# Optimization experiments

Hardware: AMD Instinct MI355X
Metric: run time of the kernel (lower is better)

Reference implementation:

```python
import jax, jax.numpy as jnp
import numpy as np

B, N, C = 4, 1370, 1024
H, DH = 16, C // 16
N_ROPE = 1369  # patch tokens covered by RoPE (prefix=1 CLS token)


def _rotate_half(x):
    x1, x2 = jnp.split(x, 2, axis=-1)
    return jnp.concatenate([-x2, x1], axis=-1)


def _rope_apply(x, sin, cos):
    return x * cos + _rotate_half(x) * sin


def setup_inputs() -> dict:
    key = jax.random.key(0)
    ks = jax.random.split(key, 7)
    return {
        "x": jax.random.normal(ks[0], (B, N, C), dtype=jnp.float32),
        "sin": jax.random.normal(ks[1], (N_ROPE, DH), dtype=jnp.float32),
        "cos": jax.random.normal(ks[2], (N_ROPE, DH), dtype=jnp.float32),
        "w_qkv": jax.random.normal(ks[3], (C, 3 * C), dtype=jnp.float32) * (C ** -0.5),
        "b_qkv": jax.random.normal(ks[4], (3 * C,), dtype=jnp.float32) * 0.02,
        "w_proj": jax.random.normal(ks[5], (C, C), dtype=jnp.float32) * (C ** -0.5),
        "b_proj": jax.random.normal(ks[6], (C,), dtype=jnp.float32) * 0.02,
    }


def reference(x, sin, cos, w_qkv, b_qkv, w_proj, b_proj):
    b, n, c = x.shape
    # QKV projection -> [3, B, H, N, DH]
    qkv = (x @ w_qkv + b_qkv).reshape(b, n, 3, H, DH).transpose(2, 0, 3, 1, 4)
    q, k, v = qkv[0], qkv[1], qkv[2]
    # RoPE on the last N_ROPE tokens (prefix tokens, e.g. CLS, left untouched)
    prefix = n - sin.shape[-2]
    q = jnp.concatenate([q[:, :, :prefix, :], _rope_apply(q[:, :, prefix:, :], sin, cos)], axis=-2)
    k = jnp.concatenate([k[:, :, :prefix, :], _rope_apply(k[:, :, prefix:, :], sin, cos)], axis=-2)
    # Full attention
    scale = 1.0 / jnp.sqrt(jnp.asarray(DH, dtype=x.dtype))
    attn = jnp.einsum('bhqd,bhkd->bhqk', q, k) * scale
    attn = jax.nn.softmax(attn, axis=-1)
    out = jnp.einsum('bhqk,bhkd->bhqd', attn, v)
    out = out.transpose(0, 2, 1, 3).reshape(b, n, c)
    return out @ w_proj + b_proj
```

## Files before the change

### kernel.cpp

```cpp
#include <hip/hip_runtime.h>
#include <hip/hip_bf16.h>

#define B_ 4
#define N_ 1370
#define C_ 1024
#define H_ 16
#define DH_ 64
#define NR_ 1369
#define M_ (B_*N_)
#define VTS_ 1408
#define ALS 64
#define PLS 72

#define QSCALE 0.1803368801111f

typedef _Float16 f16x8  __attribute__((ext_vector_type(8)));
typedef __bf16   bf16x8 __attribute__((ext_vector_type(8)));
typedef float    f32x4  __attribute__((ext_vector_type(4)));

__device__ __forceinline__ f16x8 ld_frag_h(const unsigned short* p) {
    uint4 u = *(const uint4*)p;
    return __builtin_bit_cast(f16x8, u);
}
__device__ __forceinline__ bf16x8 ld_frag_b(const unsigned short* p) {
    uint4 u = *(const uint4*)p;
    return __builtin_bit_cast(bf16x8, u);
}
__device__ __forceinline__ unsigned short f2h(float f) {
    _Float16 h = (_Float16)f;
    return __builtin_bit_cast(unsigned short, h);
}
__device__ __forceinline__ unsigned short f2bf(float f) {
    __hip_bfloat16 h = __float2bfloat16(f);
    return __builtin_bit_cast(unsigned short, h);
}
__device__ __forceinline__ bf16x8 ones_bf() {
    uint4 u = make_uint4(0x3F803F80u, 0x3F803F80u, 0x3F803F80u, 0x3F803F80u);
    return __builtin_bit_cast(bf16x8, u);
}

__device__ __forceinline__ void load_lds16(const unsigned short* g, unsigned short* l) {
    __builtin_amdgcn_global_load_lds(
        (const __attribute__((address_space(1))) unsigned int*)g,
        (__attribute__((address_space(3))) unsigned int*)l,
        16, 0, 0);
}

__global__ __launch_bounds__(256)
void conv_x_k(const float* __restrict__ x, unsigned short* __restrict__ xo, int total4) {
    int i = blockIdx.x * 256 + threadIdx.x;
    if (i >= total4) return;
    float4 v = ((const float4*)x)[i];
    ushort4 h;
    h.x = f2h(v.x); h.y = f2h(v.y); h.z = f2h(v.z); h.w = f2h(v.w);
    ((ushort4*)xo)[i] = h;
}

__global__ __launch_bounds__(256)
void conv_wt_k(const float* __restrict__ w, unsigned short* __restrict__ wt, int Ncol) {
    __shared__ unsigned short Th[64][68];
    const int tid = threadIdx.x, tx = tid & 15, ty = tid >> 4;
    const int k0 = blockIdx.y * 64, n0 = blockIdx.x * 64;
    #pragma unroll
    for (int i = 0; i < 4; ++i) {
        const int k = ty + i * 16;
        float4 v = *(const float4*)&w[(size_t)(k0 + k) * Ncol + n0 + tx * 4];
        Th[k][tx*4+0] = f2h(v.x); Th[k][tx*4+1] = f2h(v.y);
        Th[k][tx*4+2] = f2h(v.z); Th[k][tx*4+3] = f2h(v.w);
    }
    __syncthreads();
    #pragma unroll
    for (int i = 0; i < 4; ++i) {
        const int n = ty + i * 16;
        ushort4 o;
        o.x = Th[tx*4+0][n]; o.y = Th[tx*4+1][n]; o.z = Th[tx*4+2][n]; o.w = Th[tx*4+3][n];
        *(ushort4*)&wt[(size_t)(n0 + n) * 1024 + k0 + tx * 4] = o;
    }
}

__global__ __launch_bounds__(256)
void transpose_v_k(const unsigned short* __restrict__ v, unsigned short* __restrict__ vt) {
    __shared__ unsigned short Th[64][68];
    const int tid = threadIdx.x, tx = tid & 15, ty = tid >> 4;
    const int bh = blockIdx.y, t0 = blockIdx.x * 64;
    const unsigned short* vp = v + (size_t)bh * N_ * DH_;
    unsigned short* vtp = vt + (size_t)bh * DH_ * VTS_;
    #pragma unroll
    for (int i = 0; i < 4; ++i) {
        const int tok = ty + i * 16;
        const int gtok = t0 + tok;
        ushort4 val;
        if (gtok < N_) val = *(const ushort4*)&vp[(size_t)gtok * DH_ + tx * 4];
        else { val.x = 0; val.y = 0; val.z = 0; val.w = 0; }
        Th[tok][tx*4+0] = val.x; Th[tok][tx*4+1] = val.y;
        Th[tok][tx*4+2] = val.z; Th[tok][tx*4+3] = val.w;
    }
    __syncthreads();
    #pragma unroll
    for (int i = 0; i < 4; ++i) {
        const int d = ty + i * 16;
        ushort4 o;
        o.x = Th[tx*4+0][d]; o.y = Th[tx*4+1][d]; o.z = Th[tx*4+2][d]; o.w = Th[tx*4+3][d];
        *(ushort4*)&vtp[(size_t)d * VTS_ + t0 + tx * 4] = o;
    }
}

__global__ __launch_bounds__(512, 4)
void gemm_qkv8(const unsigned short* __restrict__ A, const unsigned short* __restrict__ Bt,
               const float* __restrict__ bias,
               unsigned short* __restrict__ qb, unsigned short* __restrict__ kb,
               unsigned short* __restrict__ vb,
               const float* __restrict__ sinp, const float* __restrict__ cosp)
{
    __shared__ __align__(16) unsigned short A_s[2][192 * 64];
    __shared__ __align__(16) unsigned short B_s[2][128 * 64];

    const int tid = threadIdx.x;
    const int wave = tid >> 6, lane = tid & 63;
    const int quad = lane >> 4, l16 = lane & 15;
    const int m0 = blockIdx.y * 192, n0 = blockIdx.x * 128;
    const int mwave = (wave >> 1) * 48;
    const int nwave = (wave & 1) * 64;

    const int srow = lane >> 3;
    const int gseg = (lane & 7) ^ srow;

    f32x4 acc[3][4] = {};

    auto stage = [&](int kc, int buf) {
        const int kof = kc * 64;
        #pragma unroll
        for (int i = 0; i < 3; ++i) {
            const int rbase = wave * 24 + i * 8;
            int arow = m0 + rbase + srow;
            if (arow > M_ - 1) arow = M_ - 1;
            load_lds16(A + (size_t)arow * 1024 + kof + gseg * 8, &A_s[buf][rbase * 64]);
        }
        #pragma unroll
        for (int i = 0; i < 2; ++i) {
            const int rbase = wave * 16 + i * 8;
            const int brow = n0 + rbase + srow;
            load_lds16(Bt + (size_t)brow * 1024 + kof + gseg * 8, &B_s[buf][rbase * 64]);
        }
    };

    stage(0, 0);

    for (int kc = 0; kc < 16; ++kc) {
        const int cur = kc & 1;
        __syncthreads();
        if (kc + 1 < 16) stage(kc + 1, cur ^ 1);

        #pragma unroll
        for (int kh = 0; kh < 2; ++kh) {
            const int soff = (((kh * 4 + quad) ^ (l16 & 7)) << 3);
            f16x8 a[3], b[4];
            #pragma unroll
            for (int t = 0; t < 3; ++t)
                a[t] = ld_frag_h(&A_s[cur][(mwave + t * 16 + l16) * 64 + soff]);
            #pragma unroll
            for (int t = 0; t < 4; ++t)
                b[t] = ld_frag_h(&B_s[cur][(nwave + t * 16 + l16) * 64 + soff]);
            #pragma unroll
            for (int i = 0; i < 3; ++i)
                #pragma unroll
                for (int j = 0; j < 4; ++j)
                    acc[i][j] = __builtin_amdgcn_mfma_f32_16x16x32_f16(a[i], b[j], acc[i][j], 0, 0, 0);
        }
    }

    const int nbase = n0 + nwave;
    const int part = nbase >> 10;
    const int h = (nbase & 1023) >> 6;
    #pragma unroll
    for (int i = 0; i < 3; ++i) {
        #pragma unroll
        for (int r = 0; r < 4; ++r) {
            const int gm = m0 + mwave + i * 16 + quad * 4 + r;
            if (gm >= M_) continue;
            const int b = gm / N_;
            const int tok = gm - b * N_;

            float val[4];
            #pragma unroll
            for (int j = 0; j < 4; ++j)
                val[j] = acc[i][j][r] + bias[nbase + j * 16 + l16];

            if (part < 2 && tok >= 1) {
                const float* sp = sinp + (size_t)(tok - 1) * DH_;
                const float* cp = cosp + (size_t)(tok - 1) * DH_;
                const float s0 = sp[l16],      s1 = sp[16 + l16];
                const float s2 = sp[32 + l16], s3 = sp[48 + l16];
                const float c0 = cp[l16],      c1 = cp[16 + l16];
                const float c2 = cp[32 + l16], c3 = cp[48 + l16];
                const float n0v = fmaf(val[0], c0, -val[2] * s0);
                const float n1v = fmaf(val[1], c1, -val[3] * s1);
                const float n2v = fmaf(val[2], c2,  val[0] * s2);
                const float n3v = fmaf(val[3], c3,  val[1] * s3);
                val[0] = n0v; val[1] = n1v; val[2] = n2v; val[3] = n3v;
            }

            const int bh = b * H_ + h;
            #pragma unroll
            for (int j = 0; j < 4; ++j) {
                const int d = j * 16 + l16;
                if (part == 0)      qb[((size_t)bh * N_ + tok) * DH_ + d] = f2h(val[j] * QSCALE);
                else if (part == 1) kb[((size_t)bh * N_ + tok) * DH_ + d] = f2h(val[j]);
                else                vb[((size_t)bh * N_ + tok) * DH_ + d] = f2bf(val[j]);
            }
        }
    }
}

template<int MT>
__global__ __launch_bounds__(256)
void gemm_mfma(const unsigned short* __restrict__ A, const unsigned short* __restrict__ Bt,
               const float* __restrict__ bias, float* __restrict__ out, int nchunks)
{
    constexpr int MI = MT / 32;
    __shared__ __align__(16) unsigned short A_s[MT * 64];
    __shared__ __align__(16) unsigned short B_s[128 * 64];

    const int tid = threadIdx.x;
    const int wave = tid >> 6, lane = tid & 63;
    const int quad = lane >> 4, l16 = lane & 15;
    const int m0 = blockIdx.y * MT, n0 = blockIdx.x * 128;
    const int mwave = (wave & 1) * (MT / 2), nwave = (wave >> 1) * 64;

    const int srow = lane >> 3;
    const int gseg = (lane & 7) ^ srow;

    f32x4 acc[MI][4] = {};

    for (int kc = 0; kc < nchunks; ++kc) {
        const int kof = kc * 64;

        __syncthreads();
        #pragma unroll
        for (int i = 0; i < MI; ++i) {
            const int rbase = wave * (8 * MI) + i * 8;
            int arow = m0 + rbase + srow;
            if (arow > M_ - 1) arow = M_ - 1;
            load_lds16(A + (size_t)arow * 1024 + kof + gseg * 8, &A_s[rbase * 64]);
        }
        #pragma unroll
        for (int i = 0; i < 4; ++i) {
            const int rbase = wave * 32 + i * 8;
            const int brow = n0 + rbase + srow;
            load_lds16(Bt + (size_t)brow * 1024 + kof + gseg * 8, &B_s[rbase * 64]);
        }
        __syncthreads();

        #pragma unroll
        for (int kh = 0; kh < 2; ++kh) {
            const int soff = (((kh * 4 + quad) ^ (l16 & 7)) << 3);
            f16x8 a[MI], b[4];
            #pragma unroll
            for (int t = 0; t < MI; ++t)
                a[t] = ld_frag_h(&A_s[(mwave + t * 16 + l16) * 64 + soff]);
            #pragma unroll
            for (int t = 0; t < 4; ++t)
                b[t] = ld_frag_h(&B_s[(nwave + t * 16 + l16) * 64 + soff]);
            #pragma unroll
            for (int i = 0; i < MI; ++i)
                #pragma unroll
                for (int j = 0; j < 4; ++j)
                    acc[i][j] = __builtin_amdgcn_mfma_f32_16x16x32_f16(a[i], b[j], acc[i][j], 0, 0, 0);
        }
    }

    #pragma unroll
    for (int i = 0; i < MI; ++i) {
        #pragma unroll
        for (int r = 0; r < 4; ++r) {
            const int gm = m0 + mwave + i * 16 + quad * 4 + r;
            if (gm >= M_) continue;
            #pragma unroll
            for (int j = 0; j < 4; ++j) {
                const int gn = n0 + nwave + j * 16 + l16;
                out[(size_t)gm * 1024 + gn] = acc[i][j][r] + bias[gn];
            }
        }
    }
}

__global__ __launch_bounds__(512, 6)
void attn_k(const unsigned short* __restrict__ q, const unsigned short* __restrict__ k,
            const unsigned short* __restrict__ vt, unsigned short* __restrict__ out)
{
    __shared__ __align__(16) unsigned short Ks[2][64 * ALS];
    __shared__ __align__(16) unsigned short Vs[2][64 * ALS];
    __shared__ __align__(16) unsigned short Ps[8 * 16 * PLS];

    const int tid  = threadIdx.x;
    const int wave = tid >> 6, lane = tid & 63;
    const int quad = lane >> 4, l16 = lane & 15;
    const int srow = lane >> 3;
    const int gseg = (lane & 7) ^ srow;

    const int id  = blockIdx.x;
    const int lid = (id & 7) * 88 + (id >> 3);
    const int bh  = lid / 11;
    const int q0  = (lid - bh * 11) * 128;

    const unsigned short* qp  = q  + (size_t)bh * N_ * DH_;
    const unsigned short* kp  = k  + (size_t)bh * N_ * DH_;
    const unsigned short* vtp = vt + (size_t)bh * DH_ * VTS_;

    f16x8 qf[2];
    {
        int qrow = q0 + wave * 16 + l16;
        if (qrow > N_ - 1) qrow = N_ - 1;
        qf[0] = ld_frag_h(qp + (size_t)qrow * DH_ + quad * 8);
        qf[1] = ld_frag_h(qp + (size_t)qrow * DH_ + 32 + quad * 8);
    }

    const bf16x8 onesv = ones_bf();
    f32x4 O[4] = {};
    f32x4 L = {};

    unsigned short* Pw = Ps + wave * 16 * PLS;
    const int so0 = ((quad)     ^ (l16 & 7)) << 3;
    const int so1 = ((4 + quad) ^ (l16 & 7)) << 3;

    auto stage = [&](int ch, int buf) {
        const int k0 = ch * 64;
        const int rbase = wave * 8;
        int krow = k0 + rbase + srow;
        if (krow > N_ - 1) krow = N_ - 1;
        load_lds16(kp + (size_t)krow * DH_ + gseg * 8, &Ks[buf][rbase * ALS]);
        load_lds16(vtp + (size_t)(rbase + srow) * VTS_ + k0 + gseg * 8, &Vs[buf][rbase * ALS]);
    };

    stage(0, 0);

    for (int ch = 0; ch < 22; ++ch) {
        const int k0 = ch * 64;
        const int cur = ch & 1;
        __syncthreads();
        if (ch + 1 < 22) stage(ch + 1, 1 - cur);

        f16x8 kf[4][2];
        #pragma unroll
        for (int t = 0; t < 4; ++t) {
            kf[t][0] = ld_frag_h(&Ks[cur][(t * 16 + l16) * ALS + so0]);
            kf[t][1] = ld_frag_h(&Ks[cur][(t * 16 + l16) * ALS + so1]);
        }
        f32x4 S[4];
        #pragma unroll
        for (int t = 0; t < 4; ++t) {
            f32x4 z = {};
            z = __builtin_amdgcn_mfma_f32_16x16x32_f16(qf[0], kf[t][0], z, 0, 0, 0);
            z = __builtin_amdgcn_mfma_f32_16x16x32_f16(qf[1], kf[t][1], z, 0, 0, 0);
            S[t] = z;
        }
        if (k0 + 64 > N_) {
            #pragma unroll
            for (int t = 0; t < 4; ++t) {
                if (k0 + t * 16 + l16 >= N_) {
                    S[t][0] = -1e30f; S[t][1] = -1e30f;
                    S[t][2] = -1e30f; S[t][3] = -1e30f;
                }
            }
        }

        #pragma unroll
        for (int t = 0; t < 4; ++t) {
            #pragma unroll
            for (int r = 0; r < 4; ++r) {
                const float p = __builtin_amdgcn_exp2f(S[t][r]);
                Pw[(quad * 4 + r) * PLS + t * 16 + l16] = f2bf(p);
            }
        }
        __builtin_amdgcn_wave_barrier();

        bf16x8 pf[2];
        pf[0] = ld_frag_b(&Pw[l16 * PLS + quad * 8]);
        pf[1] = ld_frag_b(&Pw[l16 * PLS + 32 + quad * 8]);

        bf16x8 vf[4][2];
        #pragma unroll
        for (int dt = 0; dt < 4; ++dt) {
            vf[dt][0] = ld_frag_b(&Vs[cur][(dt * 16 + l16) * ALS + so0]);
            vf[dt][1] = ld_frag_b(&Vs[cur][(dt * 16 + l16) * ALS + so1]);
        }
        L = __builtin_amdgcn_mfma_f32_16x16x32_bf16(pf[0], onesv, L, 0, 0, 0);
        L = __builtin_amdgcn_mfma_f32_16x16x32_bf16(pf[1], onesv, L, 0, 0, 0);
        #pragma unroll
        for (int dt = 0; dt < 4; ++dt) {
            O[dt] = __builtin_amdgcn_mfma_f32_16x16x32_bf16(pf[0], vf[dt][0], O[dt], 0, 0, 0);
            O[dt] = __builtin_amdgcn_mfma_f32_16x16x32_bf16(pf[1], vf[dt][1], O[dt], 0, 0, 0);
        }
    }

    const int b = bh >> 4, h = bh & 15;
    #pragma unroll
    for (int r = 0; r < 4; ++r) {
        const int qi = q0 + wave * 16 + quad * 4 + r;
        if (qi < N_) {
            const float inv = 1.0f / L[r];
            unsigned short* op = out + ((size_t)(b * N_ + qi)) * C_ + h * DH_ + l16;
            #pragma unroll
            for (int dt = 0; dt < 4; ++dt) op[dt * 16] = f2h(O[dt][r] * inv);
        }
    }
}

extern "C" void kernel_launch(void* const* d_in, const int* in_sizes, int n_in,
                              void* d_out, int out_size, void* d_ws, size_t ws_size,
                              hipStream_t stream) {
    const float* x      = (const float*)d_in[0];
    const float* sinp   = (const float*)d_in[1];
    const float* cosp   = (const float*)d_in[2];
    const float* w_qkv  = (const float*)d_in[3];
    const float* b_qkv  = (const float*)d_in[4];
    const float* w_proj = (const float*)d_in[5];
    const float* b_proj = (const float*)d_in[6];
    float* out = (float*)d_out;

    unsigned short* p = (unsigned short*)d_ws;
    const size_t xsz  = (size_t)M_ * C_;
    const size_t wqsz = (size_t)3 * C_ * C_;
    const size_t wpsz = (size_t)C_ * C_;
    const size_t hsz  = (size_t)B_ * H_ * N_ * DH_;
    const size_t vtsz = (size_t)B_ * H_ * DH_ * VTS_;
    unsigned short* x_h   = p;            p += xsz;
    unsigned short* wq_t  = p;            p += wqsz;
    unsigned short* wp_t  = p;            p += wpsz;
    unsigned short* q     = p;            p += hsz;
    unsigned short* k     = p;            p += hsz;
    unsigned short* vt    = p;            p += vtsz;
    unsigned short* attnb = p;            p += xsz;
    unsigned short* vb    = attnb;

    conv_x_k<<<(int)((xsz / 4 + 255) / 256), 256, 0, stream>>>(x, x_h, (int)(xsz / 4));
    conv_wt_k<<<dim3(3 * C_ / 64, C_ / 64), 256, 0, stream>>>(w_qkv, wq_t, 3 * C_);
    conv_wt_k<<<dim3(C_ / 64, C_ / 64), 256, 0, stream>>>(w_proj, wp_t, C_);

    gemm_qkv8<<<dim3(3 * C_ / 128, (M_ + 191) / 192), 512, 0, stream>>>(
        x_h, wq_t, b_qkv, q, k, vb, sinp, cosp);

    transpose_v_k<<<dim3(VTS_ / 64, B_ * H_), 256, 0, stream>>>(vb, vt);

    attn_k<<<dim3(11 * B_ * H_), 512, 0, stream>>>(q, k, vt, attnb);

    gemm_mfma<64><<<dim3(C_ / 128, (M_ + 63) / 64), 256, 0, stream>>>(
        attnb, wp_t, b_proj, out, 16);
}
```

Before: 235.0 us.

## Merge conversion kernels into one launch and double-buffer projection GEMM loads

Three preprocessing launches (x fp16 conversion and two weight transpose-converts) are combined into a single prep kernel that dispatches on block index, saving launch gaps. The output projection GEMM now uses two LDS buffers, so the next K chunk is fetched asynchronously while the current one feeds the MFMA ops, with one barrier per iteration. This doubles LDS use per block and may lower occupancy.

```diff
diff --git a/kernel.cpp b/kernel.cpp
--- a/kernel.cpp
+++ b/kernel.cpp
@@ -46,21 +46,30 @@
         16, 0, 0);
 }
 
+#define XBLK 5480
+#define WQBLK 768
+#define WPBLK 256
 __global__ __launch_bounds__(256)
-void conv_x_k(const float* __restrict__ x, unsigned short* __restrict__ xo, int total4) {
-    int i = blockIdx.x * 256 + threadIdx.x;
-    if (i >= total4) return;
-    float4 v = ((const float4*)x)[i];
-    ushort4 h;
-    h.x = f2h(v.x); h.y = f2h(v.y); h.z = f2h(v.z); h.w = f2h(v.w);
-    ((ushort4*)xo)[i] = h;
-}
-
-__global__ __launch_bounds__(256)
-void conv_wt_k(const float* __restrict__ w, unsigned short* __restrict__ wt, int Ncol) {
+void prep_k(const float* __restrict__ x, unsigned short* __restrict__ xo,
+            const float* __restrict__ wq, unsigned short* __restrict__ wqt,
+            const float* __restrict__ wp, unsigned short* __restrict__ wpt)
+{
     __shared__ unsigned short Th[64][68];
+    int bid = blockIdx.x;
+    if (bid < XBLK) {
+        const int i = bid * 256 + threadIdx.x;
+        float4 v = ((const float4*)x)[i];
+        ushort4 h;
+        h.x = f2h(v.x); h.y = f2h(v.y); h.z = f2h(v.z); h.w = f2h(v.w);
+        ((ushort4*)xo)[i] = h;
+        return;
+    }
+    bid -= XBLK;
+    const float* w; unsigned short* wt; int Ncol, nb;
+    if (bid < WQBLK) { w = wq; wt = wqt; Ncol = 3072; nb = 48; }
+    else { bid -= WQBLK; w = wp; wt = wpt; Ncol = 1024; nb = 16; }
     const int tid = threadIdx.x, tx = tid & 15, ty = tid >> 4;
-    const int k0 = blockIdx.y * 64, n0 = blockIdx.x * 64;
+    const int n0 = (bid % nb) * 64, k0 = (bid / nb) * 64;
     #pragma unroll
     for (int i = 0; i < 4; ++i) {
         const int k = ty + i * 16;
@@ -212,57 +221,60 @@
     }
 }
 
-template<int MT>
 __global__ __launch_bounds__(256)
-void gemm_mfma(const unsigned short* __restrict__ A, const unsigned short* __restrict__ Bt,
-               const float* __restrict__ bias, float* __restrict__ out, int nchunks)
+void gemm_proj2(const unsigned short* __restrict__ A, const unsigned short* __restrict__ Bt,
+                const float* __restrict__ bias, float* __restrict__ out)
 {
-    constexpr int MI = MT / 32;
-    __shared__ __align__(16) unsigned short A_s[MT * 64];
-    __shared__ __align__(16) unsigned short B_s[128 * 64];
+    __shared__ __align__(16) unsigned short A_s[2][64 * 64];
+    __shared__ __align__(16) unsigned short B_s[2][128 * 64];
 
     const int tid = threadIdx.x;
     const int wave = tid >> 6, lane = tid & 63;
     const int quad = lane >> 4, l16 = lane & 15;
-    const int m0 = blockIdx.y * MT, n0 = blockIdx.x * 128;
-    const int mwave = (wave & 1) * (MT / 2), nwave = (wave >> 1) * 64;
+    const int m0 = blockIdx.y * 64, n0 = blockIdx.x * 128;
+    const int mwave = (wave & 1) * 32, nwave = (wave >> 1) * 64;
 
     const int srow = lane >> 3;
     const int gseg = (lane & 7) ^ srow;
 
-    f32x4 acc[MI][4] = {};
-
-    for (int kc = 0; kc < nchunks; ++kc) {
+    f32x4 acc[2][4] = {};
+
+    auto stage = [&](int kc, int buf) {
         const int kof = kc * 64;
-
-        __syncthreads();
-        #pragma unroll
-        for (int i = 0; i < MI; ++i) {
-            const int rbase = wave * (8 * MI) + i * 8;
+        #pragma unroll
+        for (int i = 0; i < 2; ++i) {
+            const int rbase = wave * 16 + i * 8;
             int arow = m0 + rbase + srow;
             if (arow > M_ - 1) arow = M_ - 1;
-            load_lds16(A + (size_t)arow * 1024 + kof + gseg * 8, &A_s[rbase * 64]);
+            load_lds16(A + (size_t)arow * 1024 + kof + gseg * 8, &A_s[buf][rbase * 64]);
         }
         #pragma unroll
         for (int i = 0; i < 4; ++i) {
             const int rbase = wave * 32 + i * 8;
             const int brow = n0 + rbase + srow;
-            load_lds16(Bt + (size_t)brow * 1024 + kof + gseg * 8, &B_s[rbase * 64]);
-        }
+            load_lds16(Bt + (size_t)brow * 1024 + kof + gseg * 8, &B_s[buf][rbase * 64]);
+        }
+    };
+
+    stage(0, 0);
+
+    for (int kc = 0; kc < 16; ++kc) {
+        const int cur = kc & 1;
         __syncthreads();
+        if (kc + 1 < 16) stage(kc + 1, cur ^ 1);
 
         #pragma unroll
         for (int kh = 0; kh < 2; ++kh) {
             const int soff = (((kh * 4 + quad) ^ (l16 & 7)) << 3);
-            f16x8 a[MI], b[4];
-            #pragma unroll
-            for (int t = 0; t < MI; ++t)
-                a[t] = ld_frag_h(&A_s[(mwave + t * 16 + l16) * 64 + soff]);
+            f16x8 a[2], b[4];
+            #pragma unroll
+            for (int t = 0; t < 2; ++t)
+                a[t] = ld_frag_h(&A_s[cur][(mwave + t * 16 + l16) * 64 + soff]);
             #pragma unroll
             for (int t = 0; t < 4; ++t)
-                b[t] = ld_frag_h(&B_s[(nwave + t * 16 + l16) * 64 + soff]);
-            #pragma unroll
-            for (int i = 0; i < MI; ++i)
+                b[t] = ld_frag_h(&B_s[cur][(nwave + t * 16 + l16) * 64 + soff]);
+            #pragma unroll
+            for (int i = 0; i < 2; ++i)
                 #pragma unroll
                 for (int j = 0; j < 4; ++j)
                     acc[i][j] = __builtin_amdgcn_mfma_f32_16x16x32_f16(a[i], b[j], acc[i][j], 0, 0, 0);
@@ -270,7 +282,7 @@
     }
 
     #pragma unroll
-    for (int i = 0; i < MI; ++i) {
+    for (int i = 0; i < 2; ++i) {
         #pragma unroll
         for (int r = 0; r < 4; ++r) {
             const int gm = m0 + mwave + i * 16 + quad * 4 + r;
@@ -433,9 +445,8 @@
     unsigned short* attnb = p;            p += xsz;
     unsigned short* vb    = attnb;
 
-    conv_x_k<<<(int)((xsz / 4 + 255) / 256), 256, 0, stream>>>(x, x_h, (int)(xsz / 4));
-    conv_wt_k<<<dim3(3 * C_ / 64, C_ / 64), 256, 0, stream>>>(w_qkv, wq_t, 3 * C_);
-    conv_wt_k<<<dim3(C_ / 64, C_ / 64), 256, 0, stream>>>(w_proj, wp_t, C_);
+    prep_k<<<dim3(XBLK + WQBLK + WPBLK), 256, 0, stream>>>(
+        x, x_h, w_qkv, wq_t, w_proj, wp_t);
 
     gemm_qkv8<<<dim3(3 * C_ / 128, (M_ + 191) / 192), 512, 0, stream>>>(
         x_h, wq_t, b_qkv, q, k, vb, sinp, cosp);
@@ -444,6 +455,6 @@
 
     attn_k<<<dim3(11 * B_ * H_), 512, 0, stream>>>(q, k, vt, attnb);
 
-    gemm_mfma<64><<<dim3(C_ / 128, (M_ + 63) / 64), 256, 0, stream>>>(
-        attnb, wp_t, b_proj, out, 16);
-}
+    gemm_proj2<<<dim3(C_ / 128, (M_ + 63) / 64), 256, 0, stream>>>(
+        attnb, wp_t, b_proj, out);
+}
```

Result: faster. 230.2 us (-2.0%).
